# Kernel optimization log

Hardware: AMD Instinct MI355X
Metric: run time of the kernel (lower is better)

Reference implementation:

```python
import jax, jax.numpy as jnp
import numpy as np

B, T = 64, 2000
Q_DIM, MEM_DIM, ATT_DIM = 1024, 512, 128
N_FILTERS, KERNEL = 32, 31


def setup_inputs() -> dict:
    key = jax.random.key(0)
    ks = jax.random.split(key, 8)
    s = lambda fan_in: 1.0 / np.sqrt(fan_in)
    return {
        "attention_hidden_state": jax.random.normal(ks[0], (B, Q_DIM), jnp.float32),
        "memory": jax.random.normal(ks[1], (B, T, MEM_DIM), jnp.float32),
        "attention_weights_cat": jax.random.uniform(ks[2], (B, 2, T), jnp.float32),
        "W_query": jax.random.normal(ks[3], (Q_DIM, ATT_DIM), jnp.float32) * s(Q_DIM),
        "W_memory": jax.random.normal(ks[4], (MEM_DIM, ATT_DIM), jnp.float32) * s(MEM_DIM),
        "W_v": jax.random.normal(ks[5], (ATT_DIM, 1), jnp.float32) * s(ATT_DIM),
        "W_conv": jax.random.normal(ks[6], (KERNEL, 2, N_FILTERS), jnp.float32) * s(KERNEL * 2),  # WIO layout
        "W_loc": jax.random.normal(ks[7], (N_FILTERS, ATT_DIM), jnp.float32) * s(N_FILTERS),
    }


def reference(attention_hidden_state, memory, attention_weights_cat,
              W_query, W_memory, W_v, W_conv, W_loc):
    # processed query: [B, 1, D]
    pq = jnp.tanh(attention_hidden_state @ W_query)[:, None, :]
    # processed memory: [B, T, D]
    pm = jnp.tanh(jnp.einsum('btm,md->btd', memory, W_memory))
    # location features: Conv1D 'same', no bias, channels-last input [B, T, 2]
    awc = jnp.transpose(attention_weights_cat, (0, 2, 1))
    conv = jax.lax.conv_general_dilated(
        awc, W_conv, window_strides=(1,), padding='SAME',
        dimension_numbers=('NWC', 'WIO', 'NWC'))  # [B, T, F]
    ploc = jnp.tanh(conv @ W_loc)  # [B, T, D]
    # energies: [B, T]
    energies = jnp.squeeze(jnp.tanh(pq + ploc + pm) @ W_v, -1)
    attention_weights = jax.nn.softmax(energies, axis=1)  # [B, T]
    attention_context = jnp.einsum('bt,btm->bm', attention_weights, memory)
    return attention_context, attention_weights
```

## Files before the change

kernel.cpp:

```cpp
#include <hip/hip_runtime.h>
#include <hip/hip_bf16.h>

typedef __attribute__((ext_vector_type(8))) short s16x8;
typedef __attribute__((ext_vector_type(4))) float f32x4;

#define B_SZ 64
#define T_SZ 2000
#define QD 1024
#define MD 512
#define AD 128
#define NF 32
#define KW 31
#define NTILE 63
#define ASTRIDE 1056

__device__ __forceinline__ unsigned short f2bf(float f) {
    unsigned int u = __float_as_uint(f);
    unsigned int r = (u + 0x7FFFu + ((u >> 16) & 1u)) >> 16;
    return (unsigned short)r;
}
__device__ __forceinline__ unsigned int pack2bf_manual(float a, float b) {
    return (unsigned int)f2bf(a) | ((unsigned int)f2bf(b) << 16);
}
__device__ __forceinline__ unsigned int pack2bf(float a, float b) {
    union { __hip_bfloat162 h; unsigned int u; } cv;
    cv.h = __float22bfloat162_rn(float2{a, b});
    return cv.u;
}
__device__ __forceinline__ float fast_tanh(float x) {
    float ax = fabsf(x);
    float e = __expf(2.0f * ax);
    float r = 1.0f - 2.0f * __builtin_amdgcn_rcpf(e + 1.0f);
    return x < 0.0f ? -r : r;
}

__global__ __launch_bounds__(512) void prep_kernel(
    const float* __restrict__ ahs, const float* __restrict__ Wq,
    const float* __restrict__ Wm, const float* __restrict__ Wl,
    float* __restrict__ pq, unsigned short* __restrict__ WB,
    unsigned short* __restrict__ WL) {
    const int blk = blockIdx.x, tid = threadIdx.x;
    if (blk < 64) {
        __shared__ float q_sm[QD];
        __shared__ float part[3][AD];
        ((float2*)q_sm)[tid] = ((const float2*)(ahs + blk * QD))[tid];
        __syncthreads();
        const int d = tid & 127, kh = tid >> 7;
        const int k0 = kh * 256;
        float a0 = 0, a1 = 0, a2 = 0, a3 = 0;
        #pragma unroll 4
        for (int k = k0; k < k0 + 256; k += 4) {
            a0 += q_sm[k]     * Wq[(k)     * AD + d];
            a1 += q_sm[k + 1] * Wq[(k + 1) * AD + d];
            a2 += q_sm[k + 2] * Wq[(k + 2) * AD + d];
            a3 += q_sm[k + 3] * Wq[(k + 3) * AD + d];
        }
        float s = (a0 + a1) + (a2 + a3);
        if (kh) part[kh - 1][d] = s;
        __syncthreads();
        if (tid < AD)
            pq[blk * AD + tid] =
                fast_tanh((s + part[0][tid]) + (part[1][tid] + part[2][tid]));
    } else if (blk < 80) {
        int cidx = (blk - 64) * 512 + tid;
        int n = cidx >> 10, s = (cidx >> 6) & 15, l = cidx & 63;
        int col = n * 16 + (l & 15);
        int krow = s * 32 + (l >> 4) * 8;
        float v[8];
        #pragma unroll
        for (int j = 0; j < 8; ++j) v[j] = Wm[(krow + j) * AD + col];
        uint4 pk;
        pk.x = pack2bf(v[0], v[1]); pk.y = pack2bf(v[2], v[3]);
        pk.z = pack2bf(v[4], v[5]); pk.w = pack2bf(v[6], v[7]);
        *(uint4*)(WB + cidx * 8) = pk;
    } else {
        int cidx = tid;
        int n = cidx >> 6, l = cidx & 63;
        int col = n * 16 + (l & 15);
        int krow = (l >> 4) * 8;
        float v[8];
        #pragma unroll
        for (int j = 0; j < 8; ++j) v[j] = Wl[(krow + j) * AD + col];
        uint4 pk;
        pk.x = pack2bf_manual(v[0], v[1]); pk.y = pack2bf_manual(v[2], v[3]);
        pk.z = pack2bf_manual(v[4], v[5]); pk.w = pack2bf_manual(v[6], v[7]);
        *(uint4*)(WL + cidx * 8) = pk;
    }
}

__global__ __launch_bounds__(512, 8) void energy_kernel(
    const float* __restrict__ memory, const float* __restrict__ awcat,
    const float* __restrict__ Wconv, const float* __restrict__ Wv,
    const float* __restrict__ pq, const unsigned short* __restrict__ WB,
    const unsigned short* __restrict__ WL, float* __restrict__ wts,
    float* __restrict__ ctile, float* __restrict__ mloc,
    float* __restrict__ Stile) {
    const int tile = blockIdx.x;
    const int b = blockIdx.y;
    const int t0 = tile * 32;
    const int tid = threadIdx.x;

    __shared__ __align__(16) unsigned short Atile[32 * (ASTRIDE / 2)];
    __shared__ float aw_sm[2][64];
    __shared__ __align__(16) unsigned short conv_sm[32 * 40];
    __shared__ float e_part[32][8];
    __shared__ float e_sm[32];
    __shared__ float p_sm[32];

    {
        const float4* msrc = (const float4*)(memory + ((size_t)b * T_SZ + t0) * MD);
        #pragma unroll
        for (int it = 0; it < 4; ++it) {
            int cid = it * 512 + tid;
            int r = cid >> 6, cc = cid & 63;
            float4 v0 = {0, 0, 0, 0}, v1 = {0, 0, 0, 0};
            if (t0 + r < T_SZ) {
                v0 = msrc[r * 128 + cc * 2];
                v1 = msrc[r * 128 + cc * 2 + 1];
            }
            uint4 pk;
            pk.x = pack2bf(v0.x, v0.y); pk.y = pack2bf(v0.z, v0.w);
            pk.z = pack2bf(v1.x, v1.y); pk.w = pack2bf(v1.z, v1.w);
            int off = r * ASTRIDE + ((cc * 16) ^ ((r & 7) << 4));
            *(uint4*)((char*)Atile + off) = pk;
        }
    }

    if (tid < 128) {
        int c = tid >> 6, i = tid & 63;
        float v = 0.0f;
        int tv = t0 - 15 + i;
        if (i < 63 && tv >= 0 && tv < T_SZ) v = awcat[(b * 2 + c) * T_SZ + tv];
        aw_sm[c][i] = v;
    }
    __syncthreads();

    {
        int f = tid & 31, tq = tid >> 5;
        float acc0 = 0, acc1 = 0;
        for (int k = 0; k < KW; ++k) {
            #pragma unroll
            for (int c = 0; c < 2; ++c) {
                float wv = Wconv[(k * 2 + c) * NF + f];
                acc0 += wv * aw_sm[c][tq + k];
                acc1 += wv * aw_sm[c][tq + 16 + k];
            }
        }
        conv_sm[(tq)      * 40 + f] = f2bf(acc0);
        conv_sm[(tq + 16) * 40 + f] = f2bf(acc1);
    }
    __syncthreads();

    const int w = tid >> 6, l = tid & 63;
    const int lr = l & 15, lg = l >> 4;
    const int d = w * 16 + lr;
    const float pqv = pq[b * AD + d];
    const float wvv = Wv[d];

    f32x4 zero4 = {0, 0, 0, 0};
    f32x4 p00 = zero4, p10 = zero4;

    const s16x8* wbp = (const s16x8*)WB;
    const int swz = (lr & 7) << 4;
    const int rbase0 = lr * ASTRIDE;
    const int rbase1 = (16 + lr) * ASTRIDE;
    const int inb = lg * 16;
    const char* Ac = (const char*)Atile;

    #pragma unroll
    for (int s = 0; s < 16; ++s) {
        int j = (inb + s * 64) ^ swz;
        s16x8 a0 = *(const s16x8*)(Ac + rbase0 + j);
        s16x8 a1 = *(const s16x8*)(Ac + rbase1 + j);
        s16x8 bf = wbp[(w * 16 + s) * 64 + l];
        p00 = __builtin_amdgcn_mfma_f32_16x16x32_bf16(a0, bf, p00, 0, 0, 0);
        p10 = __builtin_amdgcn_mfma_f32_16x16x32_bf16(a1, bf, p10, 0, 0, 0);
    }

    s16x8 la0 = *(const s16x8*)((const char*)conv_sm + (lr * 80 + lg * 16));
    s16x8 la1 = *(const s16x8*)((const char*)conv_sm + ((16 + lr) * 80 + lg * 16));
    const s16x8* wlp = (const s16x8*)WL;
    s16x8 lb = wlp[w * 64 + l];
    f32x4 q00 = __builtin_amdgcn_mfma_f32_16x16x32_bf16(la0, lb, zero4, 0, 0, 0);
    f32x4 q10 = __builtin_amdgcn_mfma_f32_16x16x32_bf16(la1, lb, zero4, 0, 0, 0);

    #pragma unroll
    for (int r = 0; r < 4; ++r) {
        float v0 = fast_tanh(pqv + fast_tanh(q00[r]) + fast_tanh(p00[r])) * wvv;
        v0 += __shfl_xor(v0, 1);
        v0 += __shfl_xor(v0, 2);
        v0 += __shfl_xor(v0, 4);
        v0 += __shfl_xor(v0, 8);
        if (lr == 0) e_part[lg * 4 + r][w] = v0;
        float v1 = fast_tanh(pqv + fast_tanh(q10[r]) + fast_tanh(p10[r])) * wvv;
        v1 += __shfl_xor(v1, 1);
        v1 += __shfl_xor(v1, 2);
        v1 += __shfl_xor(v1, 4);
        v1 += __shfl_xor(v1, 8);
        if (lr == 0) e_part[16 + lg * 4 + r][w] = v1;
    }
    __syncthreads();

    if (tid < 256) {
        int t = tid >> 3, g = tid & 7;
        float v = e_part[t][g];
        v += __shfl_xor(v, 1);
        v += __shfl_xor(v, 2);
        v += __shfl_xor(v, 4);
        if (g == 0) e_sm[t] = (t0 + t < T_SZ) ? v : -3.4e38f;
    }
    __syncthreads();

    if (tid < 32) {
        int t = t0 + tid;
        bool valid = t < T_SZ;
        float e = e_sm[tid];
        float m = e;
        m = fmaxf(m, __shfl_xor(m, 1));
        m = fmaxf(m, __shfl_xor(m, 2));
        m = fmaxf(m, __shfl_xor(m, 4));
        m = fmaxf(m, __shfl_xor(m, 8));
        m = fmaxf(m, __shfl_xor(m, 16));
        float p = valid ? __expf(e - m) : 0.0f;
        p_sm[tid] = p;
        float S = p;
        S += __shfl_xor(S, 1);
        S += __shfl_xor(S, 2);
        S += __shfl_xor(S, 4);
        S += __shfl_xor(S, 8);
        S += __shfl_xor(S, 16);
        if (valid) wts[b * T_SZ + t] = p;
        if (tid == 0) { mloc[b * NTILE + tile] = m; Stile[b * NTILE + tile] = S; }
    }
    __syncthreads();

    {
        float c = 0.0f;
        const int boff = 2 * tid;
        #pragma unroll
        for (int t = 0; t < 32; ++t) {
            float p = p_sm[t];
            unsigned short us = *(const unsigned short*)(
                Ac + t * ASTRIDE + (boff ^ ((t & 7) << 4)));
            c += p * __uint_as_float(((unsigned int)us) << 16);
        }
        ctile[(((size_t)b * NTILE + tile) << 9) + tid] = c;
    }
}

__global__ __launch_bounds__(256) void finalize_kernel(
    const float* __restrict__ mloc, const float* __restrict__ Stile,
    const float* __restrict__ ctile, float* __restrict__ wts,
    float* __restrict__ ctx) {
    const int b = blockIdx.x, h = blockIdx.y, tid = threadIdx.x;
    __shared__ float sc_sm[NTILE + 1];
    if (tid < 64) {
        float m = (tid < NTILE) ? mloc[b * NTILE + tid] : -3.4e38f;
        float s = (tid < NTILE) ? Stile[b * NTILE + tid] : 0.0f;
        float M = m;
        M = fmaxf(M, __shfl_xor(M, 1));  M = fmaxf(M, __shfl_xor(M, 2));
        M = fmaxf(M, __shfl_xor(M, 4));  M = fmaxf(M, __shfl_xor(M, 8));
        M = fmaxf(M, __shfl_xor(M, 16)); M = fmaxf(M, __shfl_xor(M, 32));
        float e = __expf(m - M);
        float z = e * s;
        z += __shfl_xor(z, 1);  z += __shfl_xor(z, 2);
        z += __shfl_xor(z, 4);  z += __shfl_xor(z, 8);
        z += __shfl_xor(z, 16); z += __shfl_xor(z, 32);
        if (tid < NTILE) sc_sm[tid] = e / z;
    }
    __syncthreads();

    if (h == 0) {
        #pragma unroll
        for (int i = 0; i < 8; ++i) {
            int idx = tid + i * 256;
            if (idx < T_SZ) wts[b * T_SZ + idx] *= sc_sm[idx >> 5];
        }
    }

    float a = 0.0f;
    const float* cb = ctile + ((size_t)b * NTILE << 9) + h * 256 + tid;
    #pragma unroll 7
    for (int tl = 0; tl < NTILE; ++tl) a += sc_sm[tl] * cb[(size_t)tl << 9];
    ctx[b * MD + h * 256 + tid] = a;
}

extern "C" void kernel_launch(void* const* d_in, const int* in_sizes, int n_in,
                              void* d_out, int out_size, void* d_ws, size_t ws_size,
                              hipStream_t stream) {
    const float* ahs    = (const float*)d_in[0];
    const float* memory = (const float*)d_in[1];
    const float* awcat  = (const float*)d_in[2];
    const float* Wq     = (const float*)d_in[3];
    const float* Wm     = (const float*)d_in[4];
    const float* Wv     = (const float*)d_in[5];
    const float* Wconv  = (const float*)d_in[6];
    const float* Wl     = (const float*)d_in[7];

    float* out = (float*)d_out;
    float* ctx = out;
    float* wts = out + B_SZ * MD;

    char* ws = (char*)d_ws;
    float* pq             = (float*)(ws);
    unsigned short* WB    = (unsigned short*)(ws + 32768);
    unsigned short* WL    = (unsigned short*)(ws + 163840);
    float* mloc           = (float*)(ws + 172032);
    float* Stile          = (float*)(ws + 188160);
    float* ctile          = (float*)(ws + 204800);

    prep_kernel<<<81, 512, 0, stream>>>(ahs, Wq, Wm, Wl, pq, WB, WL);
    energy_kernel<<<dim3(NTILE, B_SZ), 512, 0, stream>>>(
        memory, awcat, Wconv, Wv, pq, WB, WL, wts, ctile, mloc, Stile);
    finalize_kernel<<<dim3(B_SZ, 2), 256, 0, stream>>>(mloc, Stile, ctile, wts, ctx);
}
```

Measured before the change: 104.9 us.

## Make energy kernel persistent over tiles with register prefetch and double-buffered LDS

Launches 4 blocks per batch row, each looping over 16 time tiles instead of one block per tile. The memory tile for the next iteration is loaded into registers while the current tile is computed, then packed into an alternate LDS buffer. Weight fragments and conv weights are loaded once per block into registers/LDS, and syncthreads are replaced with lgkmcnt waits plus barriers. This trades much lower occupancy and memory-level parallelism for reduced reload overhead and explicit overlap.

New measurement: 122.6 us. +16.9%, slower.

```diff
diff --git a/kernel.cpp b/kernel.cpp
--- a/kernel.cpp
+++ b/kernel.cpp
@@ -13,6 +13,12 @@
 #define KW 31
 #define NTILE 63
 #define ASTRIDE 1056
+#define ABUF (32 * (ASTRIDE / 2))
+
+#define LGKM_BAR() do { \
+    asm volatile("s_waitcnt lgkmcnt(0)" ::: "memory"); \
+    __builtin_amdgcn_s_barrier(); \
+} while (0)
 
 __device__ __forceinline__ unsigned short f2bf(float f) {
     unsigned int u = __float_as_uint(f);
@@ -88,163 +94,220 @@
     }
 }
 
-__global__ __launch_bounds__(512, 8) void energy_kernel(
+__global__ __launch_bounds__(512, 2) void energy_kernel(
     const float* __restrict__ memory, const float* __restrict__ awcat,
     const float* __restrict__ Wconv, const float* __restrict__ Wv,
     const float* __restrict__ pq, const unsigned short* __restrict__ WB,
     const unsigned short* __restrict__ WL, float* __restrict__ wts,
     float* __restrict__ ctile, float* __restrict__ mloc,
     float* __restrict__ Stile) {
-    const int tile = blockIdx.x;
+    const int gx = blockIdx.x;
     const int b = blockIdx.y;
-    const int t0 = tile * 32;
     const int tid = threadIdx.x;
-
-    __shared__ __align__(16) unsigned short Atile[32 * (ASTRIDE / 2)];
-    __shared__ float aw_sm[2][64];
+    const int base = gx * 16;
+    const int NT = (base + 16 <= NTILE) ? 16 : (NTILE - base);
+
+    __shared__ __align__(16) unsigned short Atile[2 * ABUF];
+    __shared__ float wconv_sm[KW * 2 * NF];
+    __shared__ float awc[2][2][64];
     __shared__ __align__(16) unsigned short conv_sm[32 * 40];
     __shared__ float e_part[32][8];
     __shared__ float e_sm[32];
     __shared__ float p_sm[32];
-
-    {
-        const float4* msrc = (const float4*)(memory + ((size_t)b * T_SZ + t0) * MD);
-        #pragma unroll
-        for (int it = 0; it < 4; ++it) {
-            int cid = it * 512 + tid;
-            int r = cid >> 6, cc = cid & 63;
-            float4 v0 = {0, 0, 0, 0}, v1 = {0, 0, 0, 0};
-            if (t0 + r < T_SZ) {
-                v0 = msrc[r * 128 + cc * 2];
-                v1 = msrc[r * 128 + cc * 2 + 1];
-            }
-            uint4 pk;
-            pk.x = pack2bf(v0.x, v0.y); pk.y = pack2bf(v0.z, v0.w);
-            pk.z = pack2bf(v1.x, v1.y); pk.w = pack2bf(v1.z, v1.w);
-            int off = r * ASTRIDE + ((cc * 16) ^ ((r & 7) << 4));
-            *(uint4*)((char*)Atile + off) = pk;
-        }
-    }
-
-    if (tid < 128) {
-        int c = tid >> 6, i = tid & 63;
-        float v = 0.0f;
-        int tv = t0 - 15 + i;
-        if (i < 63 && tv >= 0 && tv < T_SZ) v = awcat[(b * 2 + c) * T_SZ + tv];
-        aw_sm[c][i] = v;
-    }
-    __syncthreads();
-
-    {
-        int f = tid & 31, tq = tid >> 5;
-        float acc0 = 0, acc1 = 0;
-        for (int k = 0; k < KW; ++k) {
-            #pragma unroll
-            for (int c = 0; c < 2; ++c) {
-                float wv = Wconv[(k * 2 + c) * NF + f];
-                acc0 += wv * aw_sm[c][tq + k];
-                acc1 += wv * aw_sm[c][tq + 16 + k];
-            }
-        }
-        conv_sm[(tq)      * 40 + f] = f2bf(acc0);
-        conv_sm[(tq + 16) * 40 + f] = f2bf(acc1);
-    }
-    __syncthreads();
 
     const int w = tid >> 6, l = tid & 63;
     const int lr = l & 15, lg = l >> 4;
     const int d = w * 16 + lr;
     const float pqv = pq[b * AD + d];
     const float wvv = Wv[d];
-
-    f32x4 zero4 = {0, 0, 0, 0};
-    f32x4 p00 = zero4, p10 = zero4;
+    const int swz = (lr & 7) << 4;
+    const f32x4 zero4 = {0, 0, 0, 0};
 
     const s16x8* wbp = (const s16x8*)WB;
-    const int swz = (lr & 7) << 4;
-    const int rbase0 = lr * ASTRIDE;
-    const int rbase1 = (16 + lr) * ASTRIDE;
-    const int inb = lg * 16;
-    const char* Ac = (const char*)Atile;
-
+    s16x8 breg[16];
     #pragma unroll
-    for (int s = 0; s < 16; ++s) {
-        int j = (inb + s * 64) ^ swz;
-        s16x8 a0 = *(const s16x8*)(Ac + rbase0 + j);
-        s16x8 a1 = *(const s16x8*)(Ac + rbase1 + j);
-        s16x8 bf = wbp[(w * 16 + s) * 64 + l];
-        p00 = __builtin_amdgcn_mfma_f32_16x16x32_bf16(a0, bf, p00, 0, 0, 0);
-        p10 = __builtin_amdgcn_mfma_f32_16x16x32_bf16(a1, bf, p10, 0, 0, 0);
-    }
-
-    s16x8 la0 = *(const s16x8*)((const char*)conv_sm + (lr * 80 + lg * 16));
-    s16x8 la1 = *(const s16x8*)((const char*)conv_sm + ((16 + lr) * 80 + lg * 16));
-    const s16x8* wlp = (const s16x8*)WL;
-    s16x8 lb = wlp[w * 64 + l];
-    f32x4 q00 = __builtin_amdgcn_mfma_f32_16x16x32_bf16(la0, lb, zero4, 0, 0, 0);
-    f32x4 q10 = __builtin_amdgcn_mfma_f32_16x16x32_bf16(la1, lb, zero4, 0, 0, 0);
-
-    #pragma unroll
-    for (int r = 0; r < 4; ++r) {
-        float v0 = fast_tanh(pqv + fast_tanh(q00[r]) + fast_tanh(p00[r])) * wvv;
-        v0 += __shfl_xor(v0, 1);
-        v0 += __shfl_xor(v0, 2);
-        v0 += __shfl_xor(v0, 4);
-        v0 += __shfl_xor(v0, 8);
-        if (lr == 0) e_part[lg * 4 + r][w] = v0;
-        float v1 = fast_tanh(pqv + fast_tanh(q10[r]) + fast_tanh(p10[r])) * wvv;
-        v1 += __shfl_xor(v1, 1);
-        v1 += __shfl_xor(v1, 2);
-        v1 += __shfl_xor(v1, 4);
-        v1 += __shfl_xor(v1, 8);
-        if (lr == 0) e_part[16 + lg * 4 + r][w] = v1;
+    for (int s = 0; s < 16; ++s) breg[s] = wbp[(w * 16 + s) * 64 + l];
+    s16x8 lb = ((const s16x8*)WL)[w * 64 + l];
+
+    if (tid < 496) ((float4*)wconv_sm)[tid] = ((const float4*)Wconv)[tid];
+
+    {
+        const int t0 = base * 32;
+        float aw0 = 0.0f;
+        if (tid < 128) {
+            int c = tid >> 6, i = tid & 63;
+            int tv = t0 - 15 + i;
+            if (i < 63 && tv >= 0 && tv < T_SZ) aw0 = awcat[(b * 2 + c) * T_SZ + tv];
+        }
+        const float4* msrc = (const float4*)(memory + ((size_t)b * T_SZ + t0) * MD);
+        float4 v0[8];
+        #pragma unroll
+        for (int it = 0; it < 4; ++it) {
+            int cid = it * 512 + tid, r = cid >> 6, cc = cid & 63;
+            v0[2 * it]     = msrc[r * 128 + cc * 2];
+            v0[2 * it + 1] = msrc[r * 128 + cc * 2 + 1];
+        }
+        #pragma unroll
+        for (int it = 0; it < 4; ++it) {
+            int cid = it * 512 + tid, r = cid >> 6, cc = cid & 63;
+            uint4 pk;
+            pk.x = pack2bf(v0[2 * it].x, v0[2 * it].y);
+            pk.y = pack2bf(v0[2 * it].z, v0[2 * it].w);
+            pk.z = pack2bf(v0[2 * it + 1].x, v0[2 * it + 1].y);
+            pk.w = pack2bf(v0[2 * it + 1].z, v0[2 * it + 1].w);
+            *(uint4*)((char*)Atile + r * ASTRIDE + ((cc * 16) ^ ((r & 7) << 4))) = pk;
+        }
+        if (tid < 128) awc[0][tid >> 6][tid & 63] = aw0;
     }
     __syncthreads();
 
-    if (tid < 256) {
-        int t = tid >> 3, g = tid & 7;
-        float v = e_part[t][g];
-        v += __shfl_xor(v, 1);
-        v += __shfl_xor(v, 2);
-        v += __shfl_xor(v, 4);
-        if (g == 0) e_sm[t] = (t0 + t < T_SZ) ? v : -3.4e38f;
-    }
-    __syncthreads();
-
-    if (tid < 32) {
-        int t = t0 + tid;
-        bool valid = t < T_SZ;
-        float e = e_sm[tid];
-        float m = e;
-        m = fmaxf(m, __shfl_xor(m, 1));
-        m = fmaxf(m, __shfl_xor(m, 2));
-        m = fmaxf(m, __shfl_xor(m, 4));
-        m = fmaxf(m, __shfl_xor(m, 8));
-        m = fmaxf(m, __shfl_xor(m, 16));
-        float p = valid ? __expf(e - m) : 0.0f;
-        p_sm[tid] = p;
-        float S = p;
-        S += __shfl_xor(S, 1);
-        S += __shfl_xor(S, 2);
-        S += __shfl_xor(S, 4);
-        S += __shfl_xor(S, 8);
-        S += __shfl_xor(S, 16);
-        if (valid) wts[b * T_SZ + t] = p;
-        if (tid == 0) { mloc[b * NTILE + tile] = m; Stile[b * NTILE + tile] = S; }
-    }
-    __syncthreads();
-
-    {
-        float c = 0.0f;
-        const int boff = 2 * tid;
-        #pragma unroll
-        for (int t = 0; t < 32; ++t) {
-            float p = p_sm[t];
-            unsigned short us = *(const unsigned short*)(
-                Ac + t * ASTRIDE + (boff ^ ((t & 7) << 4)));
-            c += p * __uint_as_float(((unsigned int)us) << 16);
-        }
-        ctile[(((size_t)b * NTILE + tile) << 9) + tid] = c;
+    float4 v[8];
+    float aw1 = 0.0f;
+
+    for (int j = 0; j < NT; ++j) {
+        const int tile = base + j;
+        const int t0 = tile * 32;
+        const int cur = j & 1;
+        const bool hasNext = (j + 1 < NT);
+
+        if (hasNext) {
+            const int tn0 = t0 + 32;
+            aw1 = 0.0f;
+            if (tid < 128) {
+                int c = tid >> 6, i = tid & 63;
+                int tv = tn0 - 15 + i;
+                if (i < 63 && tv >= 0 && tv < T_SZ)
+                    aw1 = awcat[(b * 2 + c) * T_SZ + tv];
+            }
+            const float4* msrc =
+                (const float4*)(memory + ((size_t)b * T_SZ + tn0) * MD);
+            if (tn0 + 32 <= T_SZ) {
+                #pragma unroll
+                for (int it = 0; it < 4; ++it) {
+                    int cid = it * 512 + tid, r = cid >> 6, cc = cid & 63;
+                    v[2 * it]     = msrc[r * 128 + cc * 2];
+                    v[2 * it + 1] = msrc[r * 128 + cc * 2 + 1];
+                }
+            } else {
+                #pragma unroll
+                for (int it = 0; it < 4; ++it) {
+                    int cid = it * 512 + tid, r = cid >> 6, cc = cid & 63;
+                    float4 z = {0, 0, 0, 0};
+                    bool ok = (tn0 + r < T_SZ);
+                    v[2 * it]     = ok ? msrc[r * 128 + cc * 2]     : z;
+                    v[2 * it + 1] = ok ? msrc[r * 128 + cc * 2 + 1] : z;
+                }
+            }
+        }
+
+        {
+            int f = tid & 31, tq = tid >> 5;
+            float a0 = 0, a1 = 0;
+            for (int k = 0; k < KW; ++k) {
+                #pragma unroll
+                for (int c = 0; c < 2; ++c) {
+                    float wv = wconv_sm[(k * 2 + c) * NF + f];
+                    a0 += wv * awc[cur][c][tq + k];
+                    a1 += wv * awc[cur][c][tq + 16 + k];
+                }
+            }
+            conv_sm[(tq)      * 40 + f] = f2bf(a0);
+            conv_sm[(tq + 16) * 40 + f] = f2bf(a1);
+        }
+        LGKM_BAR();
+
+        const char* Ac = (const char*)(Atile + cur * ABUF);
+        f32x4 p00 = zero4, p10 = zero4;
+        #pragma unroll
+        for (int s = 0; s < 16; ++s) {
+            int jj = (lg * 16 + s * 64) ^ swz;
+            s16x8 a0 = *(const s16x8*)(Ac + lr * ASTRIDE + jj);
+            s16x8 a1 = *(const s16x8*)(Ac + (16 + lr) * ASTRIDE + jj);
+            p00 = __builtin_amdgcn_mfma_f32_16x16x32_bf16(a0, breg[s], p00, 0, 0, 0);
+            p10 = __builtin_amdgcn_mfma_f32_16x16x32_bf16(a1, breg[s], p10, 0, 0, 0);
+        }
+        s16x8 la0 = *(const s16x8*)((const char*)conv_sm + (lr * 80 + lg * 16));
+        s16x8 la1 = *(const s16x8*)((const char*)conv_sm + ((16 + lr) * 80 + lg * 16));
+        f32x4 q00 = __builtin_amdgcn_mfma_f32_16x16x32_bf16(la0, lb, zero4, 0, 0, 0);
+        f32x4 q10 = __builtin_amdgcn_mfma_f32_16x16x32_bf16(la1, lb, zero4, 0, 0, 0);
+
+        #pragma unroll
+        for (int r = 0; r < 4; ++r) {
+            float v0 = fast_tanh(pqv + fast_tanh(q00[r]) + fast_tanh(p00[r])) * wvv;
+            v0 += __shfl_xor(v0, 1);
+            v0 += __shfl_xor(v0, 2);
+            v0 += __shfl_xor(v0, 4);
+            v0 += __shfl_xor(v0, 8);
+            if (lr == 0) e_part[lg * 4 + r][w] = v0;
+            float v1 = fast_tanh(pqv + fast_tanh(q10[r]) + fast_tanh(p10[r])) * wvv;
+            v1 += __shfl_xor(v1, 1);
+            v1 += __shfl_xor(v1, 2);
+            v1 += __shfl_xor(v1, 4);
+            v1 += __shfl_xor(v1, 8);
+            if (lr == 0) e_part[16 + lg * 4 + r][w] = v1;
+        }
+        LGKM_BAR();
+
+        if (tid < 256) {
+            int t = tid >> 3, g = tid & 7;
+            float vv = e_part[t][g];
+            vv += __shfl_xor(vv, 1);
+            vv += __shfl_xor(vv, 2);
+            vv += __shfl_xor(vv, 4);
+            if (g == 0) e_sm[t] = (t0 + t < T_SZ) ? vv : -3.4e38f;
+        }
+        LGKM_BAR();
+
+        if (tid < 32) {
+            int t = t0 + tid;
+            bool valid = t < T_SZ;
+            float e = e_sm[tid];
+            float m = e;
+            m = fmaxf(m, __shfl_xor(m, 1));
+            m = fmaxf(m, __shfl_xor(m, 2));
+            m = fmaxf(m, __shfl_xor(m, 4));
+            m = fmaxf(m, __shfl_xor(m, 8));
+            m = fmaxf(m, __shfl_xor(m, 16));
+            float p = valid ? __expf(e - m) : 0.0f;
+            p_sm[tid] = p;
+            float S = p;
+            S += __shfl_xor(S, 1);
+            S += __shfl_xor(S, 2);
+            S += __shfl_xor(S, 4);
+            S += __shfl_xor(S, 8);
+            S += __shfl_xor(S, 16);
+            if (valid) wts[b * T_SZ + t] = p;
+            if (tid == 0) { mloc[b * NTILE + tile] = m; Stile[b * NTILE + tile] = S; }
+        }
+        LGKM_BAR();
+
+        {
+            float c = 0.0f;
+            const int boff = 2 * tid;
+            #pragma unroll
+            for (int t = 0; t < 32; ++t) {
+                unsigned short us = *(const unsigned short*)(
+                    Ac + t * ASTRIDE + (boff ^ ((t & 7) << 4)));
+                c += p_sm[t] * __uint_as_float(((unsigned int)us) << 16);
+            }
+            ctile[(((size_t)b * NTILE + tile) << 9) + tid] = c;
+        }
+
+        if (hasNext) {
+            char* An = (char*)(Atile + (cur ^ 1) * ABUF);
+            #pragma unroll
+            for (int it = 0; it < 4; ++it) {
+                int cid = it * 512 + tid, r = cid >> 6, cc = cid & 63;
+                uint4 pk;
+                pk.x = pack2bf(v[2 * it].x, v[2 * it].y);
+                pk.y = pack2bf(v[2 * it].z, v[2 * it].w);
+                pk.z = pack2bf(v[2 * it + 1].x, v[2 * it + 1].y);
+                pk.w = pack2bf(v[2 * it + 1].z, v[2 * it + 1].w);
+                *(uint4*)(An + r * ASTRIDE + ((cc * 16) ^ ((r & 7) << 4))) = pk;
+            }
+            if (tid < 128) awc[cur ^ 1][tid >> 6][tid & 63] = aw1;
+        }
+        LGKM_BAR();
     }
 }
 
@@ -310,7 +373,7 @@
     float* ctile          = (float*)(ws + 204800);
 
     prep_kernel<<<81, 512, 0, stream>>>(ahs, Wq, Wm, Wl, pq, WB, WL);
-    energy_kernel<<<dim3(NTILE, B_SZ), 512, 0, stream>>>(
+    energy_kernel<<<dim3(4, B_SZ), 512, 0, stream>>>(
         memory, awcat, Wconv, Wv, pq, WB, WL, wts, ctile, mloc, Stile);
     finalize_kernel<<<dim3(B_SZ, 2), 256, 0, stream>>>(mloc, Stile, ctile, wts, ctx);
 }
```
